# Kernel tuning notes

Hardware: AMD Instinct MI355X
Metric: run time of the kernel (lower is better)

The kernel has to match this reference:

```python
import jax, jax.numpy as jnp
import numpy as np

B, S, D = 4, 2048, 1024
NH = 16
HD = D // NH

def setup_inputs() -> dict:
    key = jax.random.key(0)
    ks = jax.random.split(key, 5)
    s = 1.0 / np.sqrt(D)
    x = jax.random.normal(ks[0], (B, S, D), dtype=jnp.float32)
    Wq = jax.random.uniform(ks[1], (D, D), jnp.float32, -s, s)
    Wk = jax.random.uniform(ks[2], (D, D), jnp.float32, -s, s)
    Wv = jax.random.uniform(ks[3], (D, D), jnp.float32, -s, s)
    Wo = jax.random.uniform(ks[4], (D, D), jnp.float32, -s, s)
    return {"x": x, "Wq": Wq, "Wk": Wk, "Wv": Wv, "Wo": Wo}

def reference(x, Wq, Wk, Wv, Wo):
    # x: [B, S, D]; W*: [D_in, D_out] stored as (out,in) torch-style -> apply x @ W.T
    def proj_heads(W):
        t = jnp.einsum('bsd,ed->bse', x, W)              # [B,S,D]
        return t.reshape(B, S, NH, HD).transpose(0, 2, 1, 3)  # [B,NH,S,HD]
    q = proj_heads(Wq)
    k = proj_heads(Wk)
    v = proj_heads(Wv)
    scale = 1.0 / jnp.sqrt(jnp.asarray(HD, dtype=x.dtype))
    scores = jnp.einsum('bhqd,bhkd->bhqk', q, k) * scale   # [B,NH,S,S]
    attn = jax.nn.softmax(scores, axis=-1)
    y = jnp.einsum('bhqk,bhkd->bhqd', attn, v)             # [B,NH,S,HD]
    y = y.transpose(0, 2, 1, 3).reshape(B, S, D)
    y = jnp.einsum('bsd,ed->bse', y, Wo)                   # out_proj, no bias
    return y
```

## Files before the change

kernel.cpp:

```cpp
#include <hip/hip_runtime.h>
#include <hip/hip_bf16.h>
#include <math.h>

#define B_  4
#define S_  2048
#define D_  1024
#define NH_ 16
#define HD_ 64

typedef __attribute__((ext_vector_type(8))) short bf16x8;
typedef __attribute__((ext_vector_type(4))) float f32x4;
typedef __attribute__((ext_vector_type(4))) uint  u32x4;

#define VMCNT(n)  asm volatile("s_waitcnt vmcnt(" #n ")" ::: "memory")
#define SCHEDB()  __builtin_amdgcn_sched_barrier(0)
#define BARRIER() __builtin_amdgcn_s_barrier()

__device__ inline ushort f2bf(float f) {
    uint u = __builtin_bit_cast(uint, f);
    uint r = (u + 0x7fffu + ((u >> 16) & 1u)) >> 16;
    return (ushort)r;
}

__device__ inline uint cvt_pk_bf16(float lo, float hi) {
    uint r;
    asm volatile("v_cvt_pk_bf16_f32 %0, %1, %2" : "=v"(r) : "v"(lo), "v"(hi));
    return r;
}

__device__ inline float exp2_raw(float x) {
    float r;
    asm volatile("v_exp_f32 %0, %1" : "=v"(r) : "v"(x));
    return r;
}

#define GLOAD_LDS(gp, lp) \
    __builtin_amdgcn_global_load_lds( \
        (const __attribute__((address_space(1))) uint32_t*)((const void*)(gp)), \
        (__attribute__((address_space(3))) uint32_t*)((void*)(lp)), 16, 0, 0)

__global__ __launch_bounds__(256) void cast_all(const float* __restrict__ x,
                                                const float* __restrict__ w0,
                                                const float* __restrict__ w1,
                                                const float* __restrict__ w2,
                                                const float* __restrict__ w3,
                                                ushort* __restrict__ xb,
                                                ushort* __restrict__ wb,
                                                int nx, int nw) {
    int i = (blockIdx.x * 256 + threadIdx.x) * 4;
    const float* src;
    ushort* dst;
    if (i < nx) {
        src = x + i;
        dst = xb + i;
    } else {
        int j = i - nx;
        int t = j >> 20;
        int off = j & (nw - 1);
        src = (t == 0 ? w0 : t == 1 ? w1 : t == 2 ? w2 : w3) + off;
        dst = wb + (size_t)t * nw + off;
    }
    float4 f = *reinterpret_cast<const float4*>(src);
    ushort4 o = {f2bf(f.x), f2bf(f.y), f2bf(f.z), f2bf(f.w)};
    *reinterpret_cast<ushort4*>(dst) = o;
}

template <int MODE>
__global__ __launch_bounds__(256) void gemm128(const ushort* __restrict__ A,
                                               const ushort* __restrict__ W,
                                               void* __restrict__ Cv,
                                               int M, int Nw, int K) {
    __shared__ ushort SH[3 * 8192];
    const int tid = threadIdx.x;

    const int gx = gridDim.x;
    const int nwg = gx * gridDim.y;
    const int f = blockIdx.y * gx + blockIdx.x;
    const int cpx = nwg >> 3;
    const int tileid = (f & 7) * cpx + (f >> 3);
    const int m0 = (tileid / gx) * 128;
    const int n0 = (tileid % gx) * 128;

    const int lane = tid & 63;
    const int w = tid >> 6;
    const int wr = (w >> 1) * 64;
    const int wc = (w & 1) * 64;
    const int fr = lane & 15;
    const int fq = lane >> 4;

    f32x4 acc[4][4] = {};

    const int srow0 = tid >> 2,          scol0 = (((tid       & 3) ^ ((srow0 >> 1) & 3)) * 8);
    const int srow1 = (tid + 256) >> 2,  scol1 = ((((tid+256) & 3) ^ ((srow1 >> 1) & 3)) * 8);

    auto STAGE = [&](int k0, int bb) {
        GLOAD_LDS(&A[(size_t)(m0 + srow0) * K + k0 + scol0], &SH[bb + tid * 8]);
        GLOAD_LDS(&W[(size_t)(n0 + srow0) * K + k0 + scol0], &SH[bb + 4096 + tid * 8]);
        GLOAD_LDS(&A[(size_t)(m0 + srow1) * K + k0 + scol1], &SH[bb + (tid + 256) * 8]);
        GLOAD_LDS(&W[(size_t)(n0 + srow1) * K + k0 + scol1], &SH[bb + 4096 + (tid + 256) * 8]);
    };
    const int rsw = ((fr >> 1) & 3);
    auto COMPUTE = [&](int bb) {
        bf16x8 af[4], bfv[4];
#pragma unroll
        for (int m = 0; m < 4; ++m)
            af[m] = *reinterpret_cast<const bf16x8*>(
                &SH[bb + (wr + m * 16 + fr) * 32 + ((fq ^ rsw) * 8)]);
#pragma unroll
        for (int n = 0; n < 4; ++n)
            bfv[n] = *reinterpret_cast<const bf16x8*>(
                &SH[bb + 4096 + (wc + n * 16 + fr) * 32 + ((fq ^ rsw) * 8)]);
        __builtin_amdgcn_s_setprio(1);
#pragma unroll
        for (int m = 0; m < 4; ++m)
#pragma unroll
            for (int n = 0; n < 4; ++n)
                acc[m][n] = __builtin_amdgcn_mfma_f32_16x16x32_bf16(af[m], bfv[n], acc[m][n], 0, 0, 0);
        __builtin_amdgcn_s_setprio(0);
    };

    const int NK = K >> 5;
    STAGE(0, 0);
    STAGE(32, 8192);
    VMCNT(4);
    BARRIER(); SCHEDB();

    int ba = 0, bbuf = 8192, bc = 16384;
    for (int t = 0; t < NK; ++t) {
        if (t + 2 < NK) { STAGE((t + 2) * 32, bc); SCHEDB(); }
        COMPUTE(ba);
        if (t + 1 < NK) {
            if (t + 2 < NK) { VMCNT(4); } else { VMCNT(0); }
            BARRIER(); SCHEDB();
        }
        int tmp = ba; ba = bbuf; bbuf = bc; bc = tmp;
    }

    if (MODE == 0) {
        const int tensor = n0 >> 10;
        ushort* C = (ushort*)Cv + (size_t)tensor * ((size_t)M * 1024);
        const float sc = (tensor == 0) ? 0.18033688011112042f : 1.0f;
        const int nb = n0 & 1023;
        if (tensor == 2) {
#pragma unroll
            for (int m = 0; m < 4; ++m)
#pragma unroll
                for (int n = 0; n < 4; ++n) {
                    int colv = nb + wc + n * 16 + fr;
                    int hh = colv >> 6, dd = colv & 63;
                    int rowb = m0 + wr + m * 16 + fq * 4;
                    int bb2 = rowb >> 11;
                    int s0 = rowb & 2047;
                    int c = s0 & 63;
                    int spb = (s0 & ~63) | (32 * (c >> 5) + 8 * ((c >> 2) & 3) +
                                            4 * ((c >> 4) & 1));
                    ushort* vt = (ushort*)C;
                    size_t base = ((size_t)(bb2 * 16 + hh) * 64 + dd) * 2048 + spb;
#pragma unroll
                    for (int r = 0; r < 4; ++r)
                        vt[base + r] = f2bf(acc[m][n][r]);
                }
        } else {
#pragma unroll
            for (int m = 0; m < 4; ++m)
#pragma unroll
                for (int n = 0; n < 4; ++n) {
                    int col = nb + wc + n * 16 + fr;
                    int rowb = m0 + wr + m * 16 + fq * 4;
#pragma unroll
                    for (int r = 0; r < 4; ++r)
                        C[(size_t)(rowb + r) * 1024 + col] = f2bf(acc[m][n][r] * sc);
                }
        }
    } else {
        float* C = (float*)Cv;
#pragma unroll
        for (int m = 0; m < 4; ++m)
#pragma unroll
            for (int n = 0; n < 4; ++n) {
                int col = n0 + wc + n * 16 + fr;
                int rowb = m0 + wr + m * 16 + fq * 4;
#pragma unroll
                for (int r = 0; r < 4; ++r)
                    C[(size_t)(rowb + r) * Nw + col] = acc[m][n][r];
            }
    }
}

__global__ __launch_bounds__(256, 4) void attn_mfma(const ushort* __restrict__ Qg,
                                                    const ushort* __restrict__ Kg,
                                                    const ushort* __restrict__ VtG,
                                                    ushort* __restrict__ Yg) {
    __shared__ ushort SH[2 * 8192];

    const int tid = threadIdx.x;
    const int lane = tid & 63;
    const int w = tid >> 6;
    const int fr = lane & 15;
    const int fq = lane >> 4;

    const int lin = blockIdx.x;
    const int qt = (lin >> 3) & 15;
    const int bh = (lin & 7) * 8 + (lin >> 7);
    const int b = bh >> 4;
    const int h = bh & 15;
    const size_t hbase = (size_t)b * (S_ * D_) + (size_t)h * HD_;
    const size_t vtbase = (size_t)bh * (64 * 2048);
    const int NT = S_ / 64;

    bf16x8 qf[2][2];
#pragma unroll
    for (int m = 0; m < 2; ++m)
#pragma unroll
        for (int kk = 0; kk < 2; ++kk)
            qf[m][kk] = *reinterpret_cast<const bf16x8*>(
                &Qg[hbase + (size_t)(qt * 128 + w * 32 + m * 16 + fr) * D_ + kk * 32 + fq * 8]);

    uint rdoff[2][4];
#pragma unroll
    for (int kk = 0; kk < 2; ++kk)
#pragma unroll
        for (int n = 0; n < 4; ++n)
            rdoff[kk][n] = (uint)((n * 16 + fr) * 64 + 8 * (((kk << 2) + fq) ^ (fr & 7)));

    const int c0i = tid, c1i = tid + 256;
    const int krow0 = c0i >> 3, kslot0 = (c0i & 7) ^ (krow0 & 7);
    const int krow1 = c1i >> 3, kslot1 = (c1i & 7) ^ (krow1 & 7);
    const int vd0 = c0i >> 3, vj0 = ((c0i & 7) ^ (vd0 & 7)) * 8;
    const int vd1 = c1i >> 3, vj1 = ((c1i & 7) ^ (vd1 & 7)) * 8;

    f32x4 oy[2][4] = {};
    f32x4 lacc[2] = {};

    const u32x4 onesu = {0x3F803F80u, 0x3F803F80u, 0x3F803F80u, 0x3F803F80u};
    const bf16x8 onesf = __builtin_bit_cast(bf16x8, onesu);

    auto STAGEK = [&](int kt, int bb) {
        GLOAD_LDS(&Kg[hbase + (size_t)(kt * 64 + krow0) * D_ + kslot0 * 8], &SH[bb + c0i * 8]);
        GLOAD_LDS(&Kg[hbase + (size_t)(kt * 64 + krow1) * D_ + kslot1 * 8], &SH[bb + c1i * 8]);
    };
    auto STAGEV = [&](int kt, int bb) {
        GLOAD_LDS(&VtG[vtbase + (size_t)vd0 * 2048 + kt * 64 + vj0], &SH[bb + 4096 + c0i * 8]);
        GLOAD_LDS(&VtG[vtbase + (size_t)vd1 * 2048 + kt * 64 + vj1], &SH[bb + 4096 + c1i * 8]);
    };
    auto QKT = [&](f32x4 (&sc)[2][4], int bb) {
#pragma unroll
        for (int m = 0; m < 2; ++m)
#pragma unroll
            for (int n = 0; n < 4; ++n) sc[m][n] = f32x4{0.f, 0.f, 0.f, 0.f};
        __builtin_amdgcn_s_setprio(1);
#pragma unroll
        for (int kk = 0; kk < 2; ++kk)
#pragma unroll
            for (int n = 0; n < 4; ++n) {
                bf16x8 kf = *reinterpret_cast<const bf16x8*>(&SH[bb + rdoff[kk][n]]);
                sc[0][n] = __builtin_amdgcn_mfma_f32_16x16x32_bf16(kf, qf[0][kk], sc[0][n], 0, 0, 0);
                sc[1][n] = __builtin_amdgcn_mfma_f32_16x16x32_bf16(kf, qf[1][kk], sc[1][n], 0, 0, 0);
            }
        __builtin_amdgcn_s_setprio(0);
    };
    auto SMPV = [&](f32x4 (&sc)[2][4], int bb) {
        uint pk[2][4][2];
#pragma unroll
        for (int m = 0; m < 2; ++m) {
#pragma unroll
            for (int n = 0; n < 4; ++n)
#pragma unroll
                for (int r = 0; r < 4; ++r)
                    sc[m][n][r] = exp2_raw(sc[m][n][r]);
#pragma unroll
            for (int n = 0; n < 4; ++n) {
                pk[m][n][0] = cvt_pk_bf16(sc[m][n][0], sc[m][n][1]);
                pk[m][n][1] = cvt_pk_bf16(sc[m][n][2], sc[m][n][3]);
            }
        }
        __builtin_amdgcn_s_setprio(1);
#pragma unroll
        for (int kk = 0; kk < 2; ++kk) {
            u32x4 a0 = {pk[0][2 * kk][0], pk[0][2 * kk][1], pk[0][2 * kk + 1][0], pk[0][2 * kk + 1][1]};
            u32x4 a1 = {pk[1][2 * kk][0], pk[1][2 * kk][1], pk[1][2 * kk + 1][0], pk[1][2 * kk + 1][1]};
            bf16x8 pf0 = __builtin_bit_cast(bf16x8, a0);
            bf16x8 pf1 = __builtin_bit_cast(bf16x8, a1);
            lacc[0] = __builtin_amdgcn_mfma_f32_16x16x32_bf16(pf0, onesf, lacc[0], 0, 0, 0);
            lacc[1] = __builtin_amdgcn_mfma_f32_16x16x32_bf16(pf1, onesf, lacc[1], 0, 0, 0);
#pragma unroll
            for (int n = 0; n < 4; ++n) {
                bf16x8 vf = *reinterpret_cast<const bf16x8*>(&SH[bb + 4096 + rdoff[kk][n]]);
                oy[0][n] = __builtin_amdgcn_mfma_f32_16x16x32_bf16(pf0, vf, oy[0][n], 0, 0, 0);
                oy[1][n] = __builtin_amdgcn_mfma_f32_16x16x32_bf16(pf1, vf, oy[1][n], 0, 0, 0);
            }
        }
        __builtin_amdgcn_s_setprio(0);
    };

    STAGEK(0, 0);
    STAGEV(0, 0);
    VMCNT(0);
    BARRIER(); SCHEDB();

    f32x4 sc[2][4];
    for (int t = 0; t < NT; ++t) {
        const int A = (t & 1) * 8192, Bb = 8192 - A;
        if (t + 1 < NT) { STAGEK(t + 1, Bb); STAGEV(t + 1, Bb); SCHEDB(); }
        QKT(sc, A);
        SMPV(sc, A);
        if (t + 1 < NT) { VMCNT(0); BARRIER(); SCHEDB(); }
    }

#pragma unroll
    for (int m = 0; m < 2; ++m) {
#pragma unroll
        for (int r = 0; r < 4; ++r) {
            float inv = 1.0f / lacc[m][r];
            int row = qt * 128 + w * 32 + m * 16 + fq * 4 + r;
#pragma unroll
            for (int n = 0; n < 4; ++n)
                Yg[hbase + (size_t)row * D_ + n * 16 + fr] = f2bf(oy[m][n][r] * inv);
        }
    }
}

extern "C" void kernel_launch(void* const* d_in, const int* in_sizes, int n_in,
                              void* d_out, int out_size, void* d_ws, size_t ws_size,
                              hipStream_t stream) {
    const float* x  = (const float*)d_in[0];
    const float* Wq = (const float*)d_in[1];
    const float* Wk = (const float*)d_in[2];
    const float* Wv = (const float*)d_in[3];
    const float* Wo = (const float*)d_in[4];
    float* out = (float*)d_out;

    const size_t nx = (size_t)B_ * S_ * D_;
    const size_t nw = (size_t)D_ * D_;

    ushort* xb = (ushort*)d_ws;
    ushort* wb = xb + nx;
    ushort* qb = wb + 4 * nw;
    ushort* kb = qb + nx;
    ushort* vt = kb + nx;
    ushort* yb = vt + nx;

    dim3 blk(256);
    const int ncast = (int)((nx + 4 * nw) / 4 / 256);
    hipLaunchKernelGGL(cast_all, dim3(ncast), blk, 0, stream,
                       x, Wq, Wk, Wv, Wo, xb, wb, (int)nx, (int)nw);

    const int M = B_ * S_;
    dim3 gqkv(3072 / 128, M / 128);
    hipLaunchKernelGGL((gemm128<0>), gqkv, blk, 0, stream, xb, wb, qb, M, 3072, D_);

    dim3 gattn(1024);
    hipLaunchKernelGGL(attn_mfma, gattn, blk, 0, stream, qb, kb, vt, yb);

    dim3 gproj(D_ / 128, M / 128);
    hipLaunchKernelGGL((gemm128<1>), gproj, blk, 0, stream, yb, wb + 3 * nw, out, M, D_, D_);
}
```

Before: 164.1 us.

## Use 256x256 tiles with 8 waves and interleaved staging for QKV GEMM

Replaces the 128x128 QKV projection GEMM with a dedicated 256x256-tile kernel using 512 threads, K-steps of 64, double-buffered LDS of 128KB, and staging of A/B halves interleaved between four MFMA phases with priority raising. The larger tile is meant to raise arithmetic intensity and cut global/LDS traffic per flop, while the interleaved schedule hides load latency behind MFMA work. The output GEMM is split into its own non-templated kernel. The trade-offs are fewer workgroups (48x... 12x32 = 384) and high register and LDS pressure that may limit occupancy.

New measurement: 166.9 us. No clear change (+1.7%).

```diff
diff --git a/kernel.cpp b/kernel.cpp
--- a/kernel.cpp
+++ b/kernel.cpp
@@ -65,11 +65,163 @@
     *reinterpret_cast<ushort4*>(dst) = o;
 }
 
-template <int MODE>
-__global__ __launch_bounds__(256) void gemm128(const ushort* __restrict__ A,
-                                               const ushort* __restrict__ W,
-                                               void* __restrict__ Cv,
-                                               int M, int Nw, int K) {
+__global__ __launch_bounds__(512, 2) void gemm256_qkv(const ushort* __restrict__ A,
+                                                      const ushort* __restrict__ W,
+                                                      ushort* __restrict__ Cv,
+                                                      int M, int K) {
+    __shared__ ushort SH[65536];
+
+    const int tid = threadIdx.x;
+    const int ww = tid >> 6;
+    const int lam = tid & 63;
+    const int wm = ww >> 2;
+    const int wn = ww & 3;
+    const int fr = lam & 15;
+    const int fq = lam >> 4;
+
+    const int gx = gridDim.x;
+    const int nwg = gx * gridDim.y;
+    const int f = blockIdx.y * gx + blockIdx.x;
+    const int cpx = nwg >> 3;
+    const int tileid = (f & 7) * cpx + (f >> 3);
+    const int m0 = (tileid / gx) * 256;
+    const int n0 = (tileid % gx) * 256;
+
+    f32x4 acc[8][4] = {};
+
+    auto STAGE_A = [&](int mh, uint bufb, int k0) {
+#pragma unroll
+        for (int l = 0; l < 2; ++l) {
+            int group = ww * 2 + l;
+            int base_row = ((group >> 3) << 7) + mh * 64 + (group & 7) * 8;
+            int row = base_row + (lam >> 3);
+            int kg = (lam & 7) ^ (lam >> 3);
+            GLOAD_LDS(&A[(size_t)(m0 + row) * K + k0 + kg * 8],
+                      &SH[bufb + base_row * 64 + lam * 8]);
+        }
+    };
+    auto STAGE_B = [&](int nh, uint bufb, int k0) {
+#pragma unroll
+        for (int l = 0; l < 2; ++l) {
+            int gg = ww * 2 + l;
+            int base_row = (gg >> 2) * 64 + nh * 32 + (gg & 3) * 8;
+            int row = base_row + (lam >> 3);
+            int kg = (lam & 7) ^ (lam >> 3);
+            GLOAD_LDS(&W[(size_t)(n0 + row) * K + k0 + kg * 8],
+                      &SH[bufb + 16384 + base_row * 64 + lam * 8]);
+        }
+    };
+    auto LOAD_AF = [&](bf16x8 (&af)[8], int mh, uint bufb) {
+#pragma unroll
+        for (int mi = 0; mi < 4; ++mi)
+#pragma unroll
+            for (int kh = 0; kh < 2; ++kh) {
+                int row = wm * 128 + (mh * 4 + mi) * 16 + fr;
+                af[mi * 2 + kh] = *reinterpret_cast<const bf16x8*>(
+                    &SH[bufb + row * 64 + ((((kh << 2) | fq) ^ (fr & 7)) << 3)]);
+            }
+    };
+    auto LOAD_BF = [&](bf16x8 (&bfv)[4], int nh, uint bufb) {
+#pragma unroll
+        for (int nn = 0; nn < 2; ++nn)
+#pragma unroll
+            for (int kh = 0; kh < 2; ++kh) {
+                int row = wn * 64 + (nh * 2 + nn) * 16 + fr;
+                bfv[nn * 2 + kh] = *reinterpret_cast<const bf16x8*>(
+                    &SH[bufb + 16384 + row * 64 + ((((kh << 2) | fq) ^ (fr & 7)) << 3)]);
+            }
+    };
+
+    bf16x8 af0[8], af1[8], bfv[4];
+
+#define MFMA16(AF, MB, NB)                                                     \
+    __builtin_amdgcn_s_setprio(1);                                             \
+    _Pragma("unroll")                                                          \
+    for (int mi = 0; mi < 4; ++mi)                                             \
+        _Pragma("unroll")                                                      \
+        for (int nn = 0; nn < 2; ++nn)                                         \
+            _Pragma("unroll")                                                  \
+            for (int kh = 0; kh < 2; ++kh)                                     \
+                acc[(MB) + mi][(NB) + nn] = __builtin_amdgcn_mfma_f32_16x16x32_bf16( \
+                    AF[mi * 2 + kh], bfv[nn * 2 + kh], acc[(MB) + mi][(NB) + nn], 0, 0, 0); \
+    __builtin_amdgcn_s_setprio(0);
+
+    const int NK = K >> 6;
+
+    STAGE_A(0, 0, 0); STAGE_A(1, 0, 0);
+    STAGE_B(0, 0, 0); STAGE_B(1, 0, 0);
+    STAGE_A(0, 32768, 64); STAGE_B(0, 32768, 64);
+    VMCNT(4);
+    BARRIER(); SCHEDB();
+
+    for (int t = 0; t < NK; ++t) {
+        const uint cur = (t & 1) * 32768u, nxt = 32768u - cur;
+        const int k1 = (t + 1) << 6, k2 = (t + 2) << 6;
+        if (t + 1 < NK) STAGE_A(1, nxt, k1);
+        LOAD_AF(af0, 0, cur);
+        LOAD_BF(bfv, 0, cur);
+        BARRIER();
+        MFMA16(af0, 0, 0);
+        BARRIER(); SCHEDB();
+        if (t + 1 < NK) STAGE_B(1, nxt, k1);
+        LOAD_AF(af1, 1, cur);
+        BARRIER();
+        MFMA16(af1, 4, 0);
+        BARRIER(); SCHEDB();
+        if (t + 2 < NK) STAGE_B(0, cur, k2);
+        LOAD_BF(bfv, 1, cur);
+        BARRIER();
+        MFMA16(af0, 0, 2);
+        BARRIER(); SCHEDB();
+        if (t + 2 < NK) STAGE_A(0, cur, k2);
+        BARRIER();
+        MFMA16(af1, 4, 2);
+        BARRIER(); SCHEDB();
+        if (t + 2 < NK) { VMCNT(4); }
+        else if (t + 1 < NK) { VMCNT(0); }
+    }
+#undef MFMA16
+
+    const int tensor = n0 >> 10;
+    ushort* C = Cv + (size_t)tensor * ((size_t)M * 1024);
+    const float scq = (tensor == 0) ? 0.18033688011112042f : 1.0f;
+    const int nb = n0 & 1023;
+    if (tensor == 2) {
+#pragma unroll
+        for (int mi = 0; mi < 8; ++mi)
+#pragma unroll
+            for (int nf = 0; nf < 4; ++nf) {
+                int colv = nb + wn * 64 + nf * 16 + fr;
+                int hh = colv >> 6, dd = colv & 63;
+                int rowb = m0 + wm * 128 + mi * 16 + fq * 4;
+                int bb2 = rowb >> 11;
+                int s0 = rowb & 2047;
+                int c = s0 & 63;
+                int spb = (s0 & ~63) | (32 * (c >> 5) + 8 * ((c >> 2) & 3) +
+                                        4 * ((c >> 4) & 1));
+                size_t base = ((size_t)(bb2 * 16 + hh) * 64 + dd) * 2048 + spb;
+#pragma unroll
+                for (int r = 0; r < 4; ++r)
+                    C[base + r] = f2bf(acc[mi][nf][r]);
+            }
+    } else {
+#pragma unroll
+        for (int mi = 0; mi < 8; ++mi)
+#pragma unroll
+            for (int nf = 0; nf < 4; ++nf) {
+                int col = nb + wn * 64 + nf * 16 + fr;
+                int rowb = m0 + wm * 128 + mi * 16 + fq * 4;
+#pragma unroll
+                for (int r = 0; r < 4; ++r)
+                    C[(size_t)(rowb + r) * 1024 + col] = f2bf(acc[mi][nf][r] * scq);
+            }
+    }
+}
+
+__global__ __launch_bounds__(256) void gemm128_out(const ushort* __restrict__ A,
+                                                   const ushort* __restrict__ W,
+                                                   float* __restrict__ C,
+                                                   int M, int Nw, int K) {
     __shared__ ushort SH[3 * 8192];
     const int tid = threadIdx.x;
 
@@ -136,55 +288,16 @@
         int tmp = ba; ba = bbuf; bbuf = bc; bc = tmp;
     }
 
-    if (MODE == 0) {
-        const int tensor = n0 >> 10;
-        ushort* C = (ushort*)Cv + (size_t)tensor * ((size_t)M * 1024);
-        const float sc = (tensor == 0) ? 0.18033688011112042f : 1.0f;
-        const int nb = n0 & 1023;
-        if (tensor == 2) {
-#pragma unroll
-            for (int m = 0; m < 4; ++m)
-#pragma unroll
-                for (int n = 0; n < 4; ++n) {
-                    int colv = nb + wc + n * 16 + fr;
-                    int hh = colv >> 6, dd = colv & 63;
-                    int rowb = m0 + wr + m * 16 + fq * 4;
-                    int bb2 = rowb >> 11;
-                    int s0 = rowb & 2047;
-                    int c = s0 & 63;
-                    int spb = (s0 & ~63) | (32 * (c >> 5) + 8 * ((c >> 2) & 3) +
-                                            4 * ((c >> 4) & 1));
-                    ushort* vt = (ushort*)C;
-                    size_t base = ((size_t)(bb2 * 16 + hh) * 64 + dd) * 2048 + spb;
-#pragma unroll
-                    for (int r = 0; r < 4; ++r)
-                        vt[base + r] = f2bf(acc[m][n][r]);
-                }
-        } else {
-#pragma unroll
-            for (int m = 0; m < 4; ++m)
-#pragma unroll
-                for (int n = 0; n < 4; ++n) {
-                    int col = nb + wc + n * 16 + fr;
-                    int rowb = m0 + wr + m * 16 + fq * 4;
-#pragma unroll
-                    for (int r = 0; r < 4; ++r)
-                        C[(size_t)(rowb + r) * 1024 + col] = f2bf(acc[m][n][r] * sc);
-                }
-        }
-    } else {
-        float* C = (float*)Cv;
-#pragma unroll
-        for (int m = 0; m < 4; ++m)
-#pragma unroll
-            for (int n = 0; n < 4; ++n) {
-                int col = n0 + wc + n * 16 + fr;
-                int rowb = m0 + wr + m * 16 + fq * 4;
-#pragma unroll
-                for (int r = 0; r < 4; ++r)
-                    C[(size_t)(rowb + r) * Nw + col] = acc[m][n][r];
-            }
-    }
+#pragma unroll
+    for (int m = 0; m < 4; ++m)
+#pragma unroll
+        for (int n = 0; n < 4; ++n) {
+            int col = n0 + wc + n * 16 + fr;
+            int rowb = m0 + wr + m * 16 + fq * 4;
+#pragma unroll
+            for (int r = 0; r < 4; ++r)
+                C[(size_t)(rowb + r) * Nw + col] = acc[m][n][r];
+        }
 }
 
 __global__ __launch_bounds__(256, 4) void attn_mfma(const ushort* __restrict__ Qg,
@@ -346,12 +459,12 @@
                        x, Wq, Wk, Wv, Wo, xb, wb, (int)nx, (int)nw);
 
     const int M = B_ * S_;
-    dim3 gqkv(3072 / 128, M / 128);
-    hipLaunchKernelGGL((gemm128<0>), gqkv, blk, 0, stream, xb, wb, qb, M, 3072, D_);
+    dim3 gqkv(3072 / 256, M / 256);
+    hipLaunchKernelGGL(gemm256_qkv, gqkv, dim3(512), 0, stream, xb, wb, qb, M, D_);
 
     dim3 gattn(1024);
     hipLaunchKernelGGL(attn_mfma, gattn, blk, 0, stream, qb, kb, vt, yb);
 
     dim3 gproj(D_ / 128, M / 128);
-    hipLaunchKernelGGL((gemm128<1>), gproj, blk, 0, stream, yb, wb + 3 * nw, out, M, D_, D_);
-}
+    hipLaunchKernelGGL(gemm128_out, gproj, blk, 0, stream, yb, wb + 3 * nw, out, M, D_, D_);
+}
```
